# Kernel optimization log

Measured on AMD Instinct MI355X. Metric: run time of the kernel, lower is better.

The kernel has to match this reference:

```python
import jax, jax.numpy as jnp
import numpy as np

B, N, D = 4, 512, 256  # batch, num_diseases, feature_dim == hidden_dim
H = 256                # hidden_dim
EPS = 1e-5

def _layernorm(x, g, b):
    m = jnp.mean(x, axis=-1, keepdims=True)
    v = jnp.mean((x - m) ** 2, axis=-1, keepdims=True)
    return (x - m) * jax.lax.rsqrt(v + EPS) * g + b

def setup_inputs() -> dict:
    key = jax.random.key(0)
    ks = jax.random.split(key, 16)
    s = 0.02
    return {
        "x": jax.random.normal(ks[0], (B, N, D), jnp.float32),
        "area_matrix": jax.random.uniform(ks[1], (B, N), jnp.float32),
        "co_occurrence": jax.random.uniform(ks[2], (N, N), jnp.float32),
        "Wq": jax.random.normal(ks[3], (H, D), jnp.float32) * s,
        "bq": jnp.zeros((H,), jnp.float32),
        "Wk": jax.random.normal(ks[4], (H, D), jnp.float32) * s,
        "bk": jnp.zeros((H,), jnp.float32),
        "Wv": jax.random.normal(ks[5], (H, D), jnp.float32) * s,
        "bv": jnp.zeros((H,), jnp.float32),
        "We1": jax.random.normal(ks[6], (H, 2), jnp.float32) * 0.5,
        "be1": jnp.zeros((H,), jnp.float32),
        "We2": jax.random.normal(ks[7], (1, H), jnp.float32) * s,
        "be2": jnp.zeros((1,), jnp.float32),
        "Wo": jax.random.normal(ks[8], (H, H), jnp.float32) * s,
        "bo": jnp.zeros((H,), jnp.float32),
        "g_ot": jnp.ones((H,), jnp.float32),
        "b_ot": jnp.zeros((H,), jnp.float32),
        "g1": jnp.ones((H,), jnp.float32),
        "b1": jnp.zeros((H,), jnp.float32),
        "g2": jnp.ones((H,), jnp.float32),
        "b2": jnp.zeros((H,), jnp.float32),
    }

def reference(x, area_matrix, co_occurrence, Wq, bq, Wk, bk, Wv, bv,
              We1, be1, We2, be2, Wo, bo, g_ot, b_ot, g1, b1, g2, b2):
    # projections: (B, N, H)
    q = jnp.einsum('bnd,hd->bnh', x, Wq) + bq
    k = jnp.einsum('bnd,hd->bnh', x, Wk) + bk
    v = jnp.einsum('bnd,hd->bnh', x, Wv) + bv
    attn_scores = jnp.einsum('bih,bjh->bij', q, k) / jnp.sqrt(jnp.float32(H))
    # edge inputs: (B, N, N, 2) = stack(broadcast area along last N, broadcast co-occ along batch)
    area = jnp.broadcast_to(area_matrix[:, :, None], (B, N, N))
    co = jnp.broadcast_to(co_occurrence[None], (B, N, N))
    edge_inputs = jnp.stack([area, co], axis=-1)
    h = jax.nn.relu(jnp.einsum('bije,he->bijh', edge_inputs, We1) + be1)
    edge_weights = jax.nn.sigmoid(jnp.einsum('bijh,oh->bijo', h, We2) + be2)[..., 0]
    attn_probs = jax.nn.softmax(attn_scores * edge_weights, axis=-1)  # dropout = identity (eval)
    out = jnp.einsum('bij,bjh->bih', attn_probs, v)
    out = _layernorm(out, g1, b1)
    out = jax.nn.relu(_layernorm(jnp.einsum('bnh,oh->bno', out, Wo) + bo, g_ot, b_ot))
    out = _layernorm(out + x, g2, b2)
    return out
```

## Files before the change

kernel.cpp:

```cpp
#include <hip/hip_runtime.h>

typedef unsigned short u16;
typedef unsigned int u32;

#define NB 4
#define NN 512
#define ND 256
#define NH 256
#define TI 4

typedef __attribute__((ext_vector_type(8))) short short8;
typedef __attribute__((ext_vector_type(4))) float f32x4;

__device__ __forceinline__ short bf(float f) {
    u32 t; __builtin_memcpy(&t, &f, 4);
    u32 r = (t + 0x7FFFu + ((t >> 16) & 1u)) >> 16;
    return (short)(u16)r;
}
__device__ __forceinline__ float blo(u32 u) {
    u32 t = u << 16; float f; __builtin_memcpy(&f, &t, 4); return f;
}
__device__ __forceinline__ float bhi(u32 u) {
    u32 t = u & 0xFFFF0000u; float f; __builtin_memcpy(&f, &t, 4); return f;
}

__device__ __forceinline__ float waveReduceSum(float v) {
#pragma unroll
    for (int o = 32; o > 0; o >>= 1) v += __shfl_down(v, o);
    return v;
}

__device__ __forceinline__ float4 blockReduce4(float4 v, float4* red4b, bool ismax) {
#pragma unroll
    for (int o = 32; o > 0; o >>= 1) {
        float4 t;
        t.x = __shfl_down(v.x, o); t.y = __shfl_down(v.y, o);
        t.z = __shfl_down(v.z, o); t.w = __shfl_down(v.w, o);
        if (ismax) {
            v.x = fmaxf(v.x, t.x); v.y = fmaxf(v.y, t.y);
            v.z = fmaxf(v.z, t.z); v.w = fmaxf(v.w, t.w);
        } else {
            v.x += t.x; v.y += t.y; v.z += t.z; v.w += t.w;
        }
    }
    int wid = threadIdx.x >> 6;
    __syncthreads();
    if ((threadIdx.x & 63) == 0) red4b[wid] = v;
    __syncthreads();
    float4 r = red4b[0];
#pragma unroll
    for (int w = 1; w < 8; ++w) {
        float4 u = red4b[w];
        if (ismax) {
            r.x = fmaxf(r.x, u.x); r.y = fmaxf(r.y, u.y);
            r.z = fmaxf(r.z, u.z); r.w = fmaxf(r.w, u.w);
        } else {
            r.x += u.x; r.y += u.y; r.z += u.z; r.w += u.w;
        }
    }
    return r;
}

__global__ __launch_bounds__(256) void qkv_mfma(
    const float* __restrict__ x,
    const float* __restrict__ Wq, const float* __restrict__ bq,
    const float* __restrict__ Wk, const float* __restrict__ bk,
    const float* __restrict__ Wv, const float* __restrict__ bv,
    const float* __restrict__ Wo,
    float* __restrict__ q, u16* __restrict__ kp, u16* __restrict__ vp,
    u16* __restrict__ wop)
{
    const int tid = threadIdx.x;
    if (blockIdx.y == 48) {
        __shared__ float t[32][33];
        const int tx = tid & 31, ty = tid >> 5;
#pragma unroll
        for (int tt2 = 0; tt2 < 2; ++tt2) {
            const int tile = blockIdx.x * 2 + tt2;
            const int bx = tile & 7, by = tile >> 3;
            __syncthreads();
#pragma unroll
            for (int k = 0; k < 4; ++k)
                t[ty + 8 * k][tx] = Wo[(size_t)(by * 32 + ty + 8 * k) * 256 + bx * 32 + tx];
            __syncthreads();
#pragma unroll
            for (int k = 0; k < 4; ++k) {
                const int d = bx * 32 + ty + 8 * k, o = by * 32 + tx;
                wop[(size_t)(d >> 1) * 512 + 2 * o + (d & 1)] = (u16)bf(t[tx][ty + 8 * k]);
            }
        }
        return;
    }

    const int lane = tid & 63, wave = tid >> 6;
    const int r0 = blockIdx.x * 64 + wave * 16;
    const int out0 = blockIdx.y * 16;
    const int which = blockIdx.y >> 4;
    const float* W   = (which == 0) ? Wq : (which == 1) ? Wk : Wv;
    const float* bia = (which == 0) ? bq : (which == 1) ? bk : bv;

    const int m = lane & 15, koff = (lane >> 4) * 8;
    const float* Ap = x + (size_t)(r0 + m) * 256 + koff;
    const float* Bp = W + (size_t)((out0 & 255) + m) * 256 + koff;

    f32x4 acc = {0.f, 0.f, 0.f, 0.f};
#pragma unroll
    for (int kb = 0; kb < 8; ++kb) {
        float4 a0 = *(const float4*)(Ap + kb * 32);
        float4 a1 = *(const float4*)(Ap + kb * 32 + 4);
        float4 b0 = *(const float4*)(Bp + kb * 32);
        float4 b1 = *(const float4*)(Bp + kb * 32 + 4);
        short8 af, bf8;
        af[0] = bf(a0.x); af[1] = bf(a0.y); af[2] = bf(a0.z); af[3] = bf(a0.w);
        af[4] = bf(a1.x); af[5] = bf(a1.y); af[6] = bf(a1.z); af[7] = bf(a1.w);
        bf8[0] = bf(b0.x); bf8[1] = bf(b0.y); bf8[2] = bf(b0.z); bf8[3] = bf(b0.w);
        bf8[4] = bf(b1.x); bf8[5] = bf(b1.y); bf8[6] = bf(b1.z); bf8[7] = bf(b1.w);
        acc = __builtin_amdgcn_mfma_f32_16x16x32_bf16(af, bf8, acc, 0, 0, 0);
    }

    const int oc = (out0 + m) & 255;
    const float bias = bia[oc];
    const int rbase = r0 + (lane >> 4) * 4;
#pragma unroll
    for (int reg = 0; reg < 4; ++reg) {
        int R = rbase + reg;
        float val = acc[reg] + bias;
        if (which == 0) {
            q[(size_t)R * 256 + oc] = val;
        } else if (which == 1) {
            const int b_ = R >> 9, n = R & 511;
            kp[((size_t)(b_ * 128 + (oc >> 1)) * 512 + n) * 2 + (oc & 1)] = (u16)bf(val);
        } else {
            vp[(size_t)R * 256 + oc] = (u16)bf(val);
        }
    }
}

__global__ __launch_bounds__(512) void fused_kernel(
    const float* __restrict__ x, const float* __restrict__ area, const float* __restrict__ co,
    const float* __restrict__ We1, const float* __restrict__ be1,
    const float* __restrict__ We2, const float* __restrict__ be2,
    const u32* __restrict__ wop32, const float* __restrict__ bo,
    const float* __restrict__ g_ot, const float* __restrict__ b_ot,
    const float* __restrict__ g1, const float* __restrict__ b1,
    const float* __restrict__ g2, const float* __restrict__ b2,
    const float* __restrict__ q, const u32* __restrict__ kp32, const u32* __restrict__ vp32,
    float* __restrict__ out)
{
    const int tid = threadIdx.x;
    const int b = blockIdx.x >> 7;
    const int i0 = (blockIdx.x & 127) << 2;
    const int lane = tid & 63, w = tid >> 6;

    __shared__ float histS[1024], histB[1024], hist2S[1024], hist2B[1024];
    __shared__ float srow[2048];
    __shared__ float4 red4b[8];
    __shared__ float sBaseS[4], sBaseB[4], redA[8], redB[8];

    const float be2f = be2[0];

    histS[tid] = 0.f; histS[tid + 512] = 0.f;
    histB[tid] = 0.f; histB[tid + 512] = 0.f;
    __syncthreads();
    {
        const int s = tid >> 7, h0 = tid & 127;
        const float a = area[b * NN + i0 + s];
        float baS = 0.f, baB = 0.f;
#pragma unroll
        for (int k = 0; k < 2; ++k) {
            const int h = h0 + 128 * k;
            const float w10 = We1[2 * h], w11 = We1[2 * h + 1];
            const float w2v = We2[h], be1v = be1[h];
            const float al = fmaf(a, w10, be1v);
            const float sl = w11 * w2v, bb = al * w2v;
            if (w11 == 0.f) {
                if (al > 0.f) baB += bb;
            } else {
                float tt = -al / w11;
                if (w11 > 0.f) {
                    if (tt <= 0.f)      { baS += sl; baB += bb; }
                    else if (tt < 1.f) {
                        int u = (int)(tt * 256.f); u = u > 255 ? 255 : u;
                        atomicAdd(&histS[s * 256 + u], sl);
                        atomicAdd(&histB[s * 256 + u], bb);
                    }
                } else {
                    if (tt >= 1.f)      { baS += sl; baB += bb; }
                    else if (tt > 0.f) {
                        baS += sl; baB += bb;
                        int u = (int)(tt * 256.f); u = u > 255 ? 255 : u;
                        atomicAdd(&histS[s * 256 + u], -sl);
                        atomicAdd(&histB[s * 256 + u], -bb);
                    }
                }
            }
        }
        float rS = waveReduceSum(baS), rB = waveReduceSum(baB);
        if (lane == 0) { redA[w] = rS; redB[w] = rB; }
    }
    __syncthreads();
    if (tid < 4) {
        sBaseS[tid] = redA[2 * tid] + redA[2 * tid + 1];
        sBaseB[tid] = redB[2 * tid] + redB[2 * tid + 1];
    }

    {
        const int s = w & 3;
        float* hp = (w < 4) ? histS : histB;
        float b0 = hp[s * 256 + 4 * lane + 0];
        float b1 = hp[s * 256 + 4 * lane + 1];
        float b2 = hp[s * 256 + 4 * lane + 2];
        float b3 = hp[s * 256 + 4 * lane + 3];
        float p0 = b0, p1 = p0 + b1, p2 = p1 + b2, p3 = p2 + b3;
        float incl = p3;
#pragma unroll
        for (int off = 1; off < 64; off <<= 1) {
            float t = __shfl_up(incl, off);
            if (lane >= off) incl += t;
        }
        float excl = incl - p3;
        hp[s * 256 + 4 * lane + 0] = p0 + excl;
        hp[s * 256 + 4 * lane + 1] = p1 + excl;
        hp[s * 256 + 4 * lane + 2] = p2 + excl;
        hp[s * 256 + 4 * lane + 3] = p3 + excl;
    }
    __syncthreads();

    float sA[TI];
    {
        const u32* kt = kp32 + (size_t)b * 128 * 512 + tid;
        const float* qb_ = q + (size_t)(b * NN + i0) * NH;
        float dot[TI] = {0.f, 0.f, 0.f, 0.f};
        for (int h = 0; h < 256; h += 4) {
            const int h2 = h >> 1;
            u32 ka = kt[(size_t)h2 * 512];
            u32 kb = kt[(size_t)(h2 + 1) * 512];
            float k0 = blo(ka), k1 = bhi(ka), k2 = blo(kb), k3 = bhi(kb);
#pragma unroll
            for (int ti = 0; ti < TI; ++ti) {
                float4 qv = *(const float4*)&qb_[ti * 256 + h];
                dot[ti] += qv.x * k0 + qv.y * k1 + qv.z * k2 + qv.w * k3;
            }
        }
#pragma unroll
        for (int ti = 0; ti < TI; ++ti) {
            float c = co[(size_t)(i0 + ti) * NN + tid];
            int u = (int)(c * 256.f); u = u > 255 ? 255 : u;
            float S = sBaseS[ti] + histS[ti * 256 + u];
            float B = sBaseB[ti] + histB[ti * 256 + u];
            float e = fmaf(c, S, B) + be2f;
            float ew = 1.f / (1.f + __expf(-e));
            sA[ti] = dot[ti] * 0.0625f * ew;
        }
    }

    {
        float4 m4 = make_float4(sA[0], sA[1], sA[2], sA[3]);
        m4 = blockReduce4(m4, red4b, true);
#pragma unroll
        for (int ti = 0; ti < TI; ++ti)
            srow[ti * 512 + tid] = __expf(sA[ti] - ((const float*)&m4)[ti]);
        __syncthreads();
    }

    {
        const int h2 = tid & 127, qtr = tid >> 7;
        float a0[TI] = {0.f, 0.f, 0.f, 0.f};
        float a1[TI] = {0.f, 0.f, 0.f, 0.f};
        const u32* vp_ = vp32 + (size_t)b * 512 * 128 + h2;
        const float4* s4p = (const float4*)srow;
        for (int j4 = qtr * 32; j4 < qtr * 32 + 32; ++j4) {
            const int jj = 4 * j4;
            u32 va = vp_[(size_t)(jj + 0) * 128];
            u32 vb = vp_[(size_t)(jj + 1) * 128];
            u32 vc = vp_[(size_t)(jj + 2) * 128];
            u32 vd = vp_[(size_t)(jj + 3) * 128];
            float la = blo(va), ha = bhi(va), lb = blo(vb), hb = bhi(vb);
            float lc = blo(vc), hc = bhi(vc), ld = blo(vd), hd = bhi(vd);
#pragma unroll
            for (int ti = 0; ti < TI; ++ti) {
                float4 p4 = s4p[ti * 128 + j4];
                a0[ti] += p4.x * la + p4.y * lb + p4.z * lc + p4.w * ld;
                a1[ti] += p4.x * ha + p4.y * hb + p4.z * hc + p4.w * hd;
            }
        }
        float2* bq_ = (float2*)((qtr == 0) ? histS : (qtr == 1) ? histB : (qtr == 2) ? hist2S : hist2B);
#pragma unroll
        for (int ti = 0; ti < TI; ++ti) bq_[ti * 128 + h2] = make_float2(a0[ti], a1[ti]);
        __syncthreads();
    }

    const int hP = tid & 255, half = tid >> 8;
    float accv[TI] = {0.f, 0.f, 0.f, 0.f};
    if (half == 0) {
#pragma unroll
        for (int ti = 0; ti < TI; ++ti)
            accv[ti] = histS[ti * 256 + hP] + histB[ti * 256 + hP]
                     + hist2S[ti * 256 + hP] + hist2B[ti * 256 + hP];
    }

    float4 t4;
    float dd[TI];
#pragma unroll
    for (int ti = 0; ti < TI; ++ti) ((float*)&t4)[ti] = (half == 0) ? accv[ti] : 0.f;
    float4 mean4 = blockReduce4(t4, red4b, false);
#pragma unroll
    for (int ti = 0; ti < TI; ++ti) {
        dd[ti] = (half == 0) ? accv[ti] - ((const float*)&mean4)[ti] * (1.f / 256.f) : 0.f;
        ((float*)&t4)[ti] = dd[ti] * dd[ti];
    }
    float4 var4 = blockReduce4(t4, red4b, false);
    if (half == 0) {
        const float g1v = g1[hP], b1v = b1[hP];
#pragma unroll
        for (int ti = 0; ti < TI; ++ti)
            srow[ti * 256 + hP] = dd[ti] * rsqrtf(((const float*)&var4)[ti] * (1.f / 256.f) + 1e-5f) * g1v + b1v;
    }
    __syncthreads();

    float acc2[TI] = {0.f, 0.f, 0.f, 0.f};
    {
        const u32* wp = wop32 + hP;
        const float4* y4p = (const float4*)srow;
        for (int d8 = half * 16; d8 < half * 16 + 16; ++d8) {
            const int d2 = 4 * d8;
            u32 w01 = wp[(size_t)(d2 + 0) * 256];
            u32 w23 = wp[(size_t)(d2 + 1) * 256];
            u32 w45 = wp[(size_t)(d2 + 2) * 256];
            u32 w67 = wp[(size_t)(d2 + 3) * 256];
            float f0 = blo(w01), f1 = bhi(w01), f2 = blo(w23), f3 = bhi(w23);
            float f4 = blo(w45), f5 = bhi(w45), f6 = blo(w67), f7 = bhi(w67);
#pragma unroll
            for (int ti = 0; ti < TI; ++ti) {
                float4 ya = y4p[ti * 64 + 2 * d8];
                float4 yb = y4p[ti * 64 + 2 * d8 + 1];
                acc2[ti] += ya.x * f0 + ya.y * f1 + ya.z * f2 + ya.w * f3
                          + yb.x * f4 + yb.y * f5 + yb.z * f6 + yb.w * f7;
            }
        }
        if (half == 1) {
#pragma unroll
            for (int ti = 0; ti < TI; ++ti) histS[ti * 256 + hP] = acc2[ti];
        }
        __syncthreads();
        if (half == 0) {
            const float bov = bo[hP];
#pragma unroll
            for (int ti = 0; ti < TI; ++ti) acc2[ti] += histS[ti * 256 + hP] + bov;
        }
    }

#pragma unroll
    for (int ti = 0; ti < TI; ++ti) ((float*)&t4)[ti] = (half == 0) ? acc2[ti] : 0.f;
    mean4 = blockReduce4(t4, red4b, false);
#pragma unroll
    for (int ti = 0; ti < TI; ++ti) {
        dd[ti] = (half == 0) ? acc2[ti] - ((const float*)&mean4)[ti] * (1.f / 256.f) : 0.f;
        ((float*)&t4)[ti] = dd[ti] * dd[ti];
    }
    var4 = blockReduce4(t4, red4b, false);
    float z[TI];
    const float gotv = (half == 0) ? g_ot[hP] : 0.f;
    const float botv = (half == 0) ? b_ot[hP] : 0.f;
#pragma unroll
    for (int ti = 0; ti < TI; ++ti)
        z[ti] = fmaxf(dd[ti] * rsqrtf(((const float*)&var4)[ti] * (1.f / 256.f) + 1e-5f) * gotv + botv, 0.f);

    float tt[TI];
#pragma unroll
    for (int ti = 0; ti < TI; ++ti) {
        tt[ti] = (half == 0) ? z[ti] + x[(size_t)(b * NN + i0 + ti) * ND + hP] : 0.f;
        ((float*)&t4)[ti] = tt[ti];
    }
    mean4 = blockReduce4(t4, red4b, false);
#pragma unroll
    for (int ti = 0; ti < TI; ++ti) {
        dd[ti] = (half == 0) ? tt[ti] - ((const float*)&mean4)[ti] * (1.f / 256.f) : 0.f;
        ((float*)&t4)[ti] = dd[ti] * dd[ti];
    }
    var4 = blockReduce4(t4, red4b, false);
    if (half == 0) {
        const float g2v = g2[hP], b2v = b2[hP];
#pragma unroll
        for (int ti = 0; ti < TI; ++ti) {
            float o = dd[ti] * rsqrtf(((const float*)&var4)[ti] * (1.f / 256.f) + 1e-5f) * g2v + b2v;
            out[(size_t)(b * NN + i0 + ti) * NH + hP] = o;
        }
    }
}

extern "C" void kernel_launch(void* const* d_in, const int* in_sizes, int n_in,
                              void* d_out, int out_size, void* d_ws, size_t ws_size,
                              hipStream_t stream) {
    const float* x    = (const float*)d_in[0];
    const float* area = (const float*)d_in[1];
    const float* co   = (const float*)d_in[2];
    const float* Wq   = (const float*)d_in[3];
    const float* bq   = (const float*)d_in[4];
    const float* Wk   = (const float*)d_in[5];
    const float* bk   = (const float*)d_in[6];
    const float* Wv   = (const float*)d_in[7];
    const float* bv   = (const float*)d_in[8];
    const float* We1  = (const float*)d_in[9];
    const float* be1  = (const float*)d_in[10];
    const float* We2  = (const float*)d_in[11];
    const float* be2  = (const float*)d_in[12];
    const float* Wo   = (const float*)d_in[13];
    const float* bo   = (const float*)d_in[14];
    const float* g_ot = (const float*)d_in[15];
    const float* b_ot = (const float*)d_in[16];
    const float* g1   = (const float*)d_in[17];
    const float* b1   = (const float*)d_in[18];
    const float* g2   = (const float*)d_in[19];
    const float* b2   = (const float*)d_in[20];

    float* q  = (float*)d_ws;
    u16*  kp  = (u16*)(q + (size_t)2048 * 256);
    u16*  vp  = kp + (size_t)4 * 128 * 512 * 2;
    u16*  wop = vp + (size_t)2048 * 256;

    qkv_mfma<<<dim3(32, 49), 256, 0, stream>>>(x, Wq, bq, Wk, bk, Wv, bv, Wo,
                                               q, kp, vp, wop);
    fused_kernel<<<NB * NN / TI, 512, 0, stream>>>(x, area, co, We1, be1, We2, be2,
                                                   (const u32*)wop, bo,
                                                   g_ot, b_ot, g1, b1, g2, b2,
                                                   q, (const u32*)kp, (const u32*)vp,
                                                   (float*)d_out);
}
```

Baseline: 167.1 us.

## Move QK^T to a separate MFMA GEMM and fuse LayerNorm reductions

The attention score dot products move out of the fused kernel's scalar loop into a new bf16 MFMA kernel, s_gemm, which writes the full score matrix to workspace. Q is now stored as bf16. The softmax no longer subtracts the row max, which saves a block reduction but can overflow exp for large scores. Each LayerNorm now gathers sum and sum of squares in one combined block reduction instead of two passes, and Wo is repacked so each thread reads it with 16-byte vector loads. The trade-off is an extra kernel launch, plus writing and re-reading a 4x512x512 fp32 score matrix.

New measurement: 158.6 us. 1.05x faster.

```diff
diff --git a/kernel.cpp b/kernel.cpp
--- a/kernel.cpp
+++ b/kernel.cpp
@@ -30,35 +30,26 @@
     return v;
 }
 
-__device__ __forceinline__ float4 blockReduce4(float4 v, float4* red4b, bool ismax) {
+__device__ __forceinline__ void blockReduce8(float4& va, float4& vb, float4* red) {
 #pragma unroll
     for (int o = 32; o > 0; o >>= 1) {
-        float4 t;
-        t.x = __shfl_down(v.x, o); t.y = __shfl_down(v.y, o);
-        t.z = __shfl_down(v.z, o); t.w = __shfl_down(v.w, o);
-        if (ismax) {
-            v.x = fmaxf(v.x, t.x); v.y = fmaxf(v.y, t.y);
-            v.z = fmaxf(v.z, t.z); v.w = fmaxf(v.w, t.w);
-        } else {
-            v.x += t.x; v.y += t.y; v.z += t.z; v.w += t.w;
-        }
+        va.x += __shfl_down(va.x, o); va.y += __shfl_down(va.y, o);
+        va.z += __shfl_down(va.z, o); va.w += __shfl_down(va.w, o);
+        vb.x += __shfl_down(vb.x, o); vb.y += __shfl_down(vb.y, o);
+        vb.z += __shfl_down(vb.z, o); vb.w += __shfl_down(vb.w, o);
     }
     int wid = threadIdx.x >> 6;
     __syncthreads();
-    if ((threadIdx.x & 63) == 0) red4b[wid] = v;
-    __syncthreads();
-    float4 r = red4b[0];
+    if ((threadIdx.x & 63) == 0) { red[2 * wid] = va; red[2 * wid + 1] = vb; }
+    __syncthreads();
+    float4 ra = red[0], rb = red[1];
 #pragma unroll
     for (int w = 1; w < 8; ++w) {
-        float4 u = red4b[w];
-        if (ismax) {
-            r.x = fmaxf(r.x, u.x); r.y = fmaxf(r.y, u.y);
-            r.z = fmaxf(r.z, u.z); r.w = fmaxf(r.w, u.w);
-        } else {
-            r.x += u.x; r.y += u.y; r.z += u.z; r.w += u.w;
-        }
-    }
-    return r;
+        float4 ua = red[2 * w], ub = red[2 * w + 1];
+        ra.x += ua.x; ra.y += ua.y; ra.z += ua.z; ra.w += ua.w;
+        rb.x += ub.x; rb.y += ub.y; rb.z += ub.z; rb.w += ub.w;
+    }
+    va = ra; vb = rb;
 }
 
 __global__ __launch_bounds__(256) void qkv_mfma(
@@ -67,7 +58,7 @@
     const float* __restrict__ Wk, const float* __restrict__ bk,
     const float* __restrict__ Wv, const float* __restrict__ bv,
     const float* __restrict__ Wo,
-    float* __restrict__ q, u16* __restrict__ kp, u16* __restrict__ vp,
+    u16* __restrict__ qb, u16* __restrict__ kb, u16* __restrict__ vp,
     u16* __restrict__ wop)
 {
     const int tid = threadIdx.x;
@@ -86,7 +77,7 @@
 #pragma unroll
             for (int k = 0; k < 4; ++k) {
                 const int d = bx * 32 + ty + 8 * k, o = by * 32 + tx;
-                wop[(size_t)(d >> 1) * 512 + 2 * o + (d & 1)] = (u16)bf(t[tx][ty + 8 * k]);
+                wop[(size_t)(d >> 3) * 2048 + o * 8 + (d & 7)] = (u16)bf(t[tx][ty + 8 * k]);
             }
         }
         return;
@@ -98,6 +89,7 @@
     const int which = blockIdx.y >> 4;
     const float* W   = (which == 0) ? Wq : (which == 1) ? Wk : Wv;
     const float* bia = (which == 0) ? bq : (which == 1) ? bk : bv;
+    u16* dst         = (which == 0) ? qb : (which == 1) ? kb : vp;
 
     const int m = lane & 15, koff = (lane >> 4) * 8;
     const float* Ap = x + (size_t)(r0 + m) * 256 + koff;
@@ -105,11 +97,11 @@
 
     f32x4 acc = {0.f, 0.f, 0.f, 0.f};
 #pragma unroll
-    for (int kb = 0; kb < 8; ++kb) {
-        float4 a0 = *(const float4*)(Ap + kb * 32);
-        float4 a1 = *(const float4*)(Ap + kb * 32 + 4);
-        float4 b0 = *(const float4*)(Bp + kb * 32);
-        float4 b1 = *(const float4*)(Bp + kb * 32 + 4);
+    for (int kb8 = 0; kb8 < 8; ++kb8) {
+        float4 a0 = *(const float4*)(Ap + kb8 * 32);
+        float4 a1 = *(const float4*)(Ap + kb8 * 32 + 4);
+        float4 b0 = *(const float4*)(Bp + kb8 * 32);
+        float4 b1 = *(const float4*)(Bp + kb8 * 32 + 4);
         short8 af, bf8;
         af[0] = bf(a0.x); af[1] = bf(a0.y); af[2] = bf(a0.z); af[3] = bf(a0.w);
         af[4] = bf(a1.x); af[5] = bf(a1.y); af[6] = bf(a1.z); af[7] = bf(a1.w);
@@ -124,16 +116,33 @@
 #pragma unroll
     for (int reg = 0; reg < 4; ++reg) {
         int R = rbase + reg;
-        float val = acc[reg] + bias;
-        if (which == 0) {
-            q[(size_t)R * 256 + oc] = val;
-        } else if (which == 1) {
-            const int b_ = R >> 9, n = R & 511;
-            kp[((size_t)(b_ * 128 + (oc >> 1)) * 512 + n) * 2 + (oc & 1)] = (u16)bf(val);
-        } else {
-            vp[(size_t)R * 256 + oc] = (u16)bf(val);
-        }
-    }
+        dst[(size_t)R * 256 + oc] = (u16)bf(acc[reg] + bias);
+    }
+}
+
+__global__ __launch_bounds__(256) void s_gemm(
+    const u16* __restrict__ qb, const u16* __restrict__ kb, float* __restrict__ S)
+{
+    const int lane = threadIdx.x & 63, wave = threadIdx.x >> 6;
+    const int job = blockIdx.x * 4 + wave;
+    const int b = job >> 10, rem = job & 1023;
+    const int i0 = (rem >> 5) * 16, j0 = (rem & 31) * 16;
+    const int m = lane & 15, koff = (lane >> 4) * 8;
+    const u16* Ap = qb + (size_t)(b * 512 + i0 + m) * 256 + koff;
+    const u16* Bp = kb + (size_t)(b * 512 + j0 + m) * 256 + koff;
+
+    f32x4 acc = {0.f, 0.f, 0.f, 0.f};
+#pragma unroll
+    for (int kb8 = 0; kb8 < 8; ++kb8) {
+        short8 a  = *(const short8*)(Ap + kb8 * 32);
+        short8 bf8 = *(const short8*)(Bp + kb8 * 32);
+        acc = __builtin_amdgcn_mfma_f32_16x16x32_bf16(a, bf8, acc, 0, 0, 0);
+    }
+    const int col = j0 + m;
+    const int rbase = i0 + (lane >> 4) * 4;
+#pragma unroll
+    for (int reg = 0; reg < 4; ++reg)
+        S[(size_t)(b * 512 + rbase + reg) * 512 + col] = acc[reg];
 }
 
 __global__ __launch_bounds__(512) void fused_kernel(
@@ -144,7 +153,7 @@
     const float* __restrict__ g_ot, const float* __restrict__ b_ot,
     const float* __restrict__ g1, const float* __restrict__ b1,
     const float* __restrict__ g2, const float* __restrict__ b2,
-    const float* __restrict__ q, const u32* __restrict__ kp32, const u32* __restrict__ vp32,
+    const float* __restrict__ S, const u32* __restrict__ vp32,
     float* __restrict__ out)
 {
     const int tid = threadIdx.x;
@@ -154,7 +163,7 @@
 
     __shared__ float histS[1024], histB[1024], hist2S[1024], hist2B[1024];
     __shared__ float srow[2048];
-    __shared__ float4 red4b[8];
+    __shared__ float4 red8b[16];
     __shared__ float sBaseS[4], sBaseB[4], redA[8], redB[8];
 
     const float be2f = be2[0];
@@ -226,40 +235,18 @@
     }
     __syncthreads();
 
-    float sA[TI];
     {
-        const u32* kt = kp32 + (size_t)b * 128 * 512 + tid;
-        const float* qb_ = q + (size_t)(b * NN + i0) * NH;
-        float dot[TI] = {0.f, 0.f, 0.f, 0.f};
-        for (int h = 0; h < 256; h += 4) {
-            const int h2 = h >> 1;
-            u32 ka = kt[(size_t)h2 * 512];
-            u32 kb = kt[(size_t)(h2 + 1) * 512];
-            float k0 = blo(ka), k1 = bhi(ka), k2 = blo(kb), k3 = bhi(kb);
-#pragma unroll
-            for (int ti = 0; ti < TI; ++ti) {
-                float4 qv = *(const float4*)&qb_[ti * 256 + h];
-                dot[ti] += qv.x * k0 + qv.y * k1 + qv.z * k2 + qv.w * k3;
-            }
-        }
+        const float* Sp = S + (size_t)(b * NN + i0) * 512 + tid;
 #pragma unroll
         for (int ti = 0; ti < TI; ++ti) {
             float c = co[(size_t)(i0 + ti) * NN + tid];
             int u = (int)(c * 256.f); u = u > 255 ? 255 : u;
-            float S = sBaseS[ti] + histS[ti * 256 + u];
-            float B = sBaseB[ti] + histB[ti * 256 + u];
-            float e = fmaf(c, S, B) + be2f;
+            float Sg = sBaseS[ti] + histS[ti * 256 + u];
+            float Bg = sBaseB[ti] + histB[ti * 256 + u];
+            float e = fmaf(c, Sg, Bg) + be2f;
             float ew = 1.f / (1.f + __expf(-e));
-            sA[ti] = dot[ti] * 0.0625f * ew;
-        }
-    }
-
-    {
-        float4 m4 = make_float4(sA[0], sA[1], sA[2], sA[3]);
-        m4 = blockReduce4(m4, red4b, true);
-#pragma unroll
-        for (int ti = 0; ti < TI; ++ti)
-            srow[ti * 512 + tid] = __expf(sA[ti] - ((const float*)&m4)[ti]);
+            srow[ti * 512 + tid] = __expf(Sp[(size_t)ti * 512] * 0.0625f * ew);
+        }
         __syncthreads();
     }
 
@@ -299,41 +286,36 @@
                      + hist2S[ti * 256 + hP] + hist2B[ti * 256 + hP];
     }
 
-    float4 t4;
+    float4 sa, sb;
     float dd[TI];
 #pragma unroll
-    for (int ti = 0; ti < TI; ++ti) ((float*)&t4)[ti] = (half == 0) ? accv[ti] : 0.f;
-    float4 mean4 = blockReduce4(t4, red4b, false);
-#pragma unroll
     for (int ti = 0; ti < TI; ++ti) {
-        dd[ti] = (half == 0) ? accv[ti] - ((const float*)&mean4)[ti] * (1.f / 256.f) : 0.f;
-        ((float*)&t4)[ti] = dd[ti] * dd[ti];
-    }
-    float4 var4 = blockReduce4(t4, red4b, false);
+        float v = (half == 0) ? accv[ti] : 0.f;
+        ((float*)&sa)[ti] = v; ((float*)&sb)[ti] = v * v;
+    }
+    blockReduce8(sa, sb, red8b);
     if (half == 0) {
         const float g1v = g1[hP], b1v = b1[hP];
 #pragma unroll
-        for (int ti = 0; ti < TI; ++ti)
-            srow[ti * 256 + hP] = dd[ti] * rsqrtf(((const float*)&var4)[ti] * (1.f / 256.f) + 1e-5f) * g1v + b1v;
+        for (int ti = 0; ti < TI; ++ti) {
+            float mean = ((const float*)&sa)[ti] * (1.f / 256.f);
+            float var = fmaxf(((const float*)&sb)[ti] * (1.f / 256.f) - mean * mean, 0.f);
+            srow[ti * 256 + hP] = (accv[ti] - mean) * rsqrtf(var + 1e-5f) * g1v + b1v;
+        }
     }
     __syncthreads();
 
     float acc2[TI] = {0.f, 0.f, 0.f, 0.f};
     {
-        const u32* wp = wop32 + hP;
         const float4* y4p = (const float4*)srow;
-        for (int d8 = half * 16; d8 < half * 16 + 16; ++d8) {
-            const int d2 = 4 * d8;
-            u32 w01 = wp[(size_t)(d2 + 0) * 256];
-            u32 w23 = wp[(size_t)(d2 + 1) * 256];
-            u32 w45 = wp[(size_t)(d2 + 2) * 256];
-            u32 w67 = wp[(size_t)(d2 + 3) * 256];
-            float f0 = blo(w01), f1 = bhi(w01), f2 = blo(w23), f3 = bhi(w23);
-            float f4 = blo(w45), f5 = bhi(w45), f6 = blo(w67), f7 = bhi(w67);
+        for (int g = half * 16; g < half * 16 + 16; ++g) {
+            uint4 ww = *(const uint4*)(wop32 + (size_t)g * 1024 + hP * 4);
+            float f0 = blo(ww.x), f1 = bhi(ww.x), f2 = blo(ww.y), f3 = bhi(ww.y);
+            float f4 = blo(ww.z), f5 = bhi(ww.z), f6 = blo(ww.w), f7 = bhi(ww.w);
 #pragma unroll
             for (int ti = 0; ti < TI; ++ti) {
-                float4 ya = y4p[ti * 64 + 2 * d8];
-                float4 yb = y4p[ti * 64 + 2 * d8 + 1];
+                float4 ya = y4p[ti * 64 + 2 * g];
+                float4 yb = y4p[ti * 64 + 2 * g + 1];
                 acc2[ti] += ya.x * f0 + ya.y * f1 + ya.z * f2 + ya.w * f3
                           + yb.x * f4 + yb.y * f5 + yb.z * f6 + yb.w * f7;
             }
@@ -351,39 +333,36 @@
     }
 
 #pragma unroll
-    for (int ti = 0; ti < TI; ++ti) ((float*)&t4)[ti] = (half == 0) ? acc2[ti] : 0.f;
-    mean4 = blockReduce4(t4, red4b, false);
-#pragma unroll
     for (int ti = 0; ti < TI; ++ti) {
-        dd[ti] = (half == 0) ? acc2[ti] - ((const float*)&mean4)[ti] * (1.f / 256.f) : 0.f;
-        ((float*)&t4)[ti] = dd[ti] * dd[ti];
-    }
-    var4 = blockReduce4(t4, red4b, false);
+        float v = (half == 0) ? acc2[ti] : 0.f;
+        ((float*)&sa)[ti] = v; ((float*)&sb)[ti] = v * v;
+    }
+    blockReduce8(sa, sb, red8b);
     float z[TI];
     const float gotv = (half == 0) ? g_ot[hP] : 0.f;
     const float botv = (half == 0) ? b_ot[hP] : 0.f;
 #pragma unroll
-    for (int ti = 0; ti < TI; ++ti)
-        z[ti] = fmaxf(dd[ti] * rsqrtf(((const float*)&var4)[ti] * (1.f / 256.f) + 1e-5f) * gotv + botv, 0.f);
+    for (int ti = 0; ti < TI; ++ti) {
+        float mean = ((const float*)&sa)[ti] * (1.f / 256.f);
+        float var = fmaxf(((const float*)&sb)[ti] * (1.f / 256.f) - mean * mean, 0.f);
+        dd[ti] = (half == 0) ? acc2[ti] - mean : 0.f;
+        z[ti] = fmaxf(dd[ti] * rsqrtf(var + 1e-5f) * gotv + botv, 0.f);
+    }
 
     float tt[TI];
 #pragma unroll
     for (int ti = 0; ti < TI; ++ti) {
         tt[ti] = (half == 0) ? z[ti] + x[(size_t)(b * NN + i0 + ti) * ND + hP] : 0.f;
-        ((float*)&t4)[ti] = tt[ti];
-    }
-    mean4 = blockReduce4(t4, red4b, false);
-#pragma unroll
-    for (int ti = 0; ti < TI; ++ti) {
-        dd[ti] = (half == 0) ? tt[ti] - ((const float*)&mean4)[ti] * (1.f / 256.f) : 0.f;
-        ((float*)&t4)[ti] = dd[ti] * dd[ti];
-    }
-    var4 = blockReduce4(t4, red4b, false);
+        ((float*)&sa)[ti] = tt[ti]; ((float*)&sb)[ti] = tt[ti] * tt[ti];
+    }
+    blockReduce8(sa, sb, red8b);
     if (half == 0) {
         const float g2v = g2[hP], b2v = b2[hP];
 #pragma unroll
         for (int ti = 0; ti < TI; ++ti) {
-            float o = dd[ti] * rsqrtf(((const float*)&var4)[ti] * (1.f / 256.f) + 1e-5f) * g2v + b2v;
+            float mean = ((const float*)&sa)[ti] * (1.f / 256.f);
+            float var = fmaxf(((const float*)&sb)[ti] * (1.f / 256.f) - mean * mean, 0.f);
+            float o = (tt[ti] - mean) * rsqrtf(var + 1e-5f) * g2v + b2v;
             out[(size_t)(b * NN + i0 + ti) * NH + hP] = o;
         }
     }
@@ -414,16 +393,18 @@
     const float* g2   = (const float*)d_in[19];
     const float* b2   = (const float*)d_in[20];
 
-    float* q  = (float*)d_ws;
-    u16*  kp  = (u16*)(q + (size_t)2048 * 256);
-    u16*  vp  = kp + (size_t)4 * 128 * 512 * 2;
+    u16*  qb  = (u16*)d_ws;
+    u16*  kb  = qb + (size_t)2048 * 256;
+    u16*  vp  = kb + (size_t)2048 * 256;
     u16*  wop = vp + (size_t)2048 * 256;
+    float* S  = (float*)(wop + 65536);
 
     qkv_mfma<<<dim3(32, 49), 256, 0, stream>>>(x, Wq, bq, Wk, bk, Wv, bv, Wo,
-                                               q, kp, vp, wop);
+                                               qb, kb, vp, wop);
+    s_gemm<<<1024, 256, 0, stream>>>(qb, kb, S);
     fused_kernel<<<NB * NN / TI, 512, 0, stream>>>(x, area, co, We1, be1, We2, be2,
                                                    (const u32*)wop, bo,
                                                    g_ot, b_ot, g1, b1, g2, b2,
-                                                   q, (const u32*)kp, (const u32*)vp,
+                                                   S, (const u32*)vp,
                                                    (float*)d_out);
 }
```
